# Performance work log

Hardware: AMD Instinct MI355X
Metric: run time of the kernel (lower is better)

Reference implementation:

```python
import jax, jax.numpy as jnp
import numpy as np

N, E, IN, H, NEX, NCAT = 100000, 1600000, 165, 128, 50, 3
EPS = 1e-5


def setup_inputs() -> dict:
    key = jax.random.key(0)
    ks = jax.random.split(key, 12)
    rn = lambda k, shp: (jax.random.normal(k, shp, jnp.float32) * 0.05)
    x = jax.random.normal(ks[0], (N, IN), jnp.float32)
    edge_index = jax.random.randint(ks[1], (2, E), 0, N, jnp.int32)
    inp = {
        'x': x, 'edge_index': edge_index,
        # GCN convs
        'W1': rn(ks[2], (IN, H)), 'b1': jnp.zeros((H,), jnp.float32),
        'W2': rn(ks[3], (H, H)), 'b2': jnp.zeros((H,), jnp.float32),
        # backbone BN (train-mode batch stats)
        'g1': jnp.ones((H,), jnp.float32), 'be1': jnp.zeros((H,), jnp.float32),
        'g2': jnp.ones((H,), jnp.float32), 'be2': jnp.zeros((H,), jnp.float32),
        # forward head
        'fW1': rn(ks[4], (H, H)), 'fb1': jnp.zeros((H,), jnp.float32),
        'fg1': jnp.ones((H,), jnp.float32), 'fbe1': jnp.zeros((H,), jnp.float32),
        'fW2': rn(ks[5], (H, H // 2)), 'fb2': jnp.zeros((H // 2,), jnp.float32),
        'fg2': jnp.ones((H // 2,), jnp.float32), 'fbe2': jnp.zeros((H // 2,), jnp.float32),
        'fW3': rn(ks[6], (H // 2, NEX)), 'fb3': jnp.zeros((NEX,), jnp.float32),
        # backward head
        'bW1': rn(ks[7], (H, H // 2)), 'bb1': jnp.zeros((H // 2,), jnp.float32),
        'bg1': jnp.ones((H // 2,), jnp.float32), 'bbe1': jnp.zeros((H // 2,), jnp.float32),
        'bW2': rn(ks[8], (H // 2, NCAT)), 'bb2': jnp.zeros((NCAT,), jnp.float32),
    }
    return inp


def _bn(h, g, b):
    # BatchNorm1d, training-mode stats (biased variance), dropout treated as identity
    m = h.mean(0)
    v = ((h - m) ** 2).mean(0)
    return (h - m) * jax.lax.rsqrt(v + EPS) * g + b


def _gcn(h, W, b, src, dst, dinv, n):
    h = h @ W                                   # [N, out]
    coef = (dinv[src] * dinv[dst])[:, None]     # sym-normalized edge weights
    msg = h[src] * coef                         # [E+N, out] gather
    out = jax.ops.segment_sum(msg, dst, num_segments=n)  # scatter-add
    return out + b


def reference(x, edge_index, W1, b1, W2, b2, g1, be1, g2, be2,
              fW1, fb1, fg1, fbe1, fW2, fb2, fg2, fbe2, fW3, fb3,
              bW1, bb1, bg1, bbe1, bW2, bb2):
    n = x.shape[0]
    loop = jnp.arange(n, dtype=edge_index.dtype)
    src = jnp.concatenate([edge_index[0], loop])  # add self-loops (PyG default)
    dst = jnp.concatenate([edge_index[1], loop])
    deg = jax.ops.segment_sum(jnp.ones(src.shape, x.dtype), dst, num_segments=n)
    dinv = jnp.where(deg > 0, jax.lax.rsqrt(jnp.maximum(deg, 1.0)), 0.0)

    h = jax.nn.relu(_bn(_gcn(x, W1, b1, src, dst, dinv, n), g1, be1))
    h = jax.nn.relu(_bn(_gcn(h, W2, b2, src, dst, dinv, n), g2, be2))
    emb = h

    f = jax.nn.relu(_bn(emb @ fW1 + fb1, fg1, fbe1))
    f = jax.nn.relu(_bn(f @ fW2 + fb2, fg2, fbe2))
    forward_logits = f @ fW3 + fb3

    bwd = jax.nn.relu(_bn(emb @ bW1 + bb1, bg1, bbe1))
    backward_logits = bwd @ bW2 + bb2

    return forward_logits, backward_logits, emb
```

## Files before the change

kernel.cpp:

```cpp
#include <hip/hip_runtime.h>
#include <stdint.h>

constexpr int NN = 100000;
constexpr int NE = 1600000;
constexpr int DIN = 165;
constexpr int PSZ = 12500;
constexpr int CAP = 48;

typedef __attribute__((ext_vector_type(8))) short bh8;
typedef __attribute__((ext_vector_type(4))) float f4;
typedef __attribute__((ext_vector_type(4))) float fx4;

__device__ inline unsigned short f2bf(float x) {
  union { float f; uint32_t u; } un; un.f = x;
  uint32_t u = un.u;
  return (unsigned short)((u + 0x7FFFu + ((u >> 16) & 1u)) >> 16);
}
__device__ inline float bf2f(unsigned short u) {
  union { uint32_t i; float f; } c; c.i = (uint32_t)u << 16; return c.f;
}
__device__ inline float bflo(uint32_t v) {
  union { uint32_t i; float f; } c; c.i = v << 16; return c.f;
}
__device__ inline float bfhi(uint32_t v) {
  union { uint32_t i; float f; } c; c.i = v & 0xffff0000u; return c.f;
}

__device__ inline f4 mfma16(bh8 a, bh8 b, f4 c) {
  return __builtin_amdgcn_mfma_f32_16x16x32_bf16(a, b, c, 0, 0, 0);
}

constexpr size_t OFF_DEG    = 0;
constexpr size_t OFF_STATS  = 400128;
constexpr size_t ZERO_BYTES = OFF_STATS + (size_t)5*64*256*4;
constexpr size_t OFF_DINV   = ZERO_BYTES;
constexpr size_t OFF_SS     = OFF_DINV + 400128;
constexpr size_t OFF_W1T    = OFF_SS + 5*256*4;
constexpr size_t OFF_W2T    = OFF_W1T + 128*192*2;
constexpr size_t OFF_FW1T   = OFF_W2T + 128*128*2;
constexpr size_t OFF_FW2T   = OFF_FW1T + 128*128*2;
constexpr size_t OFF_FW3T   = OFF_FW2T + 64*128*2;
constexpr size_t OFF_BW1T   = OFF_FW3T + 64*64*2;
constexpr size_t OFF_BW2T   = OFF_BW1T + 64*128*2;
constexpr size_t OFF_COL    = (OFF_BW2T + 16*64*2 + 255) & ~(size_t)255;
constexpr size_t OFF_BUF0   = (OFF_COL + (size_t)NN*CAP*4 + 255) & ~(size_t)255;
constexpr size_t OFF_BUF1   = OFF_BUF0 + (size_t)NN*128*2;
constexpr size_t OFF_BUF2   = OFF_BUF1 + (size_t)NN*128*2;

__global__ __launch_bounds__(256) void k_bfill(const int* __restrict__ srcv, const int* __restrict__ dstv,
                                               int* __restrict__ deg, int* __restrict__ colv) {
  int part = blockIdx.x & 7;
  int lo = part * PSZ, hi = lo + PSZ;
  const int4* s4 = (const int4*)srcv;
  const int4* d4 = (const int4*)dstv;
  constexpr int NQ = NE / 4;
  int stride = (gridDim.x >> 3) * 256;
#pragma unroll 2
  for (int q = (blockIdx.x >> 3) * 256 + threadIdx.x; q < NQ; q += stride) {
    int4 dd = d4[q];
    int4 ss = s4[q];
    if (dd.x >= lo && dd.x < hi) { int p = atomicAdd(&deg[dd.x], 1); if (p < CAP) colv[dd.x * CAP + p] = ss.x; }
    if (dd.y >= lo && dd.y < hi) { int p = atomicAdd(&deg[dd.y], 1); if (p < CAP) colv[dd.y * CAP + p] = ss.y; }
    if (dd.z >= lo && dd.z < hi) { int p = atomicAdd(&deg[dd.z], 1); if (p < CAP) colv[dd.z * CAP + p] = ss.z; }
    if (dd.w >= lo && dd.w < hi) { int p = atomicAdd(&deg[dd.w], 1); if (p < CAP) colv[dd.w * CAP + p] = ss.w; }
  }
}

__global__ __launch_bounds__(256) void k_prep(const float* __restrict__ W1, const float* __restrict__ W2,
                                              const float* __restrict__ fW1, const float* __restrict__ fW2,
                                              const float* __restrict__ fW3, const float* __restrict__ bW1,
                                              const float* __restrict__ bW2, char* __restrict__ wsb,
                                              const int* __restrict__ deg, float* __restrict__ dinv) {
  int b = blockIdx.x, t = threadIdx.x;
  if (b >= 308) {
    int i = (b - 308) * 256 + t;
    if (i < NN) dinv[i] = rsqrtf((float)(deg[i] + 1));
    return;
  }
  const float* src; unsigned short* dst; int K, C, Kpad, base;
  if (b < 96)       { src = W1;  dst = (unsigned short*)(wsb + OFF_W1T);  K = DIN; C = 128; Kpad = 192; base = b; }
  else if (b < 160) { src = W2;  dst = (unsigned short*)(wsb + OFF_W2T);  K = 128; C = 128; Kpad = 128; base = b - 96; }
  else if (b < 224) { src = fW1; dst = (unsigned short*)(wsb + OFF_FW1T); K = 128; C = 128; Kpad = 128; base = b - 160; }
  else if (b < 256) { src = fW2; dst = (unsigned short*)(wsb + OFF_FW2T); K = 128; C = 64;  Kpad = 128; base = b - 224; }
  else if (b < 272) { src = fW3; dst = (unsigned short*)(wsb + OFF_FW3T); K = 64;  C = 50;  Kpad = 64;  base = b - 256; }
  else if (b < 304) { src = bW1; dst = (unsigned short*)(wsb + OFF_BW1T); K = 128; C = 64;  Kpad = 128; base = b - 272; }
  else              { src = bW2; dst = (unsigned short*)(wsb + OFF_BW2T); K = 64;  C = 3;   Kpad = 64;  base = b - 304; }
  int idx = base * 256 + t;
  int c = idx / Kpad, k = idx - c * Kpad;
  float v = (c < C && k < K) ? src[k * C + c] : 0.f;
  dst[idx] = f2bf(v);
}

__global__ __launch_bounds__(256) void k_gx(const float* __restrict__ x,
                                            const unsigned short* __restrict__ W1T,
                                            unsigned short* __restrict__ out) {
  constexpr int KL = 200;
  __shared__ __attribute__((aligned(16))) unsigned short Alds[64 * KL];
  int tid = threadIdx.x;
  int lane = tid & 63, wave = tid >> 6;
  int lr = lane & 15, lk = (lane >> 4) * 8;
  int rowbase = blockIdx.x * 64;

  bh8 bw[2][6];
#pragma unroll
  for (int ct = 0; ct < 2; ++ct)
#pragma unroll
    for (int kt = 0; kt < 6; ++kt)
      bw[ct][kt] = *(const bh8*)&W1T[((wave * 2 + ct) * 16 + lr) * 192 + kt * 32 + lk];

  size_t slab = (size_t)rowbase * DIN;
  long rem = (long)NN * DIN - (long)slab;
  int lim4 = rem >= 10560 ? 2640 : (int)(rem >> 2);
  for (int z = tid; z < 64 * (192 - DIN); z += 256) {
    int r = z / (192 - DIN), k = DIN + (z - r * (192 - DIN));
    Alds[r * KL + k] = 0;
  }
  float4 regs[11];
#pragma unroll
  for (int i = 0; i < 11; ++i) {
    int idx4 = tid + i * 256;
    if (idx4 < lim4) regs[i] = *(const float4*)(x + slab + (size_t)idx4 * 4);
  }
#pragma unroll
  for (int i = 0; i < 11; ++i) {
    int idx4 = tid + i * 256;
    if (idx4 < lim4) {
      int e = idx4 * 4;
      int r = e / DIN, k = e - r * DIN;
      float vv[4] = {regs[i].x, regs[i].y, regs[i].z, regs[i].w};
#pragma unroll
      for (int j = 0; j < 4; ++j) {
        Alds[r * KL + k] = f2bf(vv[j]);
        if (++k == DIN) { k = 0; ++r; }
      }
    }
  }
  __syncthreads();

  f4 acc[4][2] = {};
  for (int kt = 0; kt < 6; ++kt) {
    bh8 a[4];
#pragma unroll
    for (int rt = 0; rt < 4; ++rt)
      a[rt] = *(const bh8*)&Alds[(rt * 16 + lr) * KL + kt * 32 + lk];
#pragma unroll
    for (int rt = 0; rt < 4; ++rt) {
      acc[rt][0] = mfma16(a[rt], bw[0][kt], acc[rt][0]);
      acc[rt][1] = mfma16(a[rt], bw[1][kt], acc[rt][1]);
    }
  }
#pragma unroll
  for (int ct = 0; ct < 2; ++ct) {
    int c = (wave * 2 + ct) * 16 + lr;
#pragma unroll
    for (int rt = 0; rt < 4; ++rt) {
      int gr0 = rowbase + rt * 16 + (lane >> 4) * 4;
#pragma unroll
      for (int rg = 0; rg < 4; ++rg) {
        int gr = gr0 + rg;
        if (gr < NN) out[(size_t)gr * 128 + c] = f2bf(acc[rt][ct][rg]);
      }
    }
  }
}

template <int KPAD, int CPAD, bool OUTBF>
__global__ __launch_bounds__(256) void k_gemm(const unsigned short* __restrict__ in, int K, int C,
                                              const float* __restrict__ ss,
                                              const unsigned short* __restrict__ WT,
                                              const float* __restrict__ bias,
                                              void* __restrict__ out_, float* __restrict__ stats) {
  constexpr int KL = KPAD + 8;
  constexpr int NKT = KPAD / 32;
  constexpr int NCTW = (CPAD >= 64) ? CPAD / 64 : 1;
  __shared__ __attribute__((aligned(16))) unsigned short Alds[64 * KL];
  __shared__ float s_sum[128], s_sq[128], sss[256];
  int tid = threadIdx.x;
  int lane = tid & 63, wave = tid >> 6;
  int lr = lane & 15, lk = (lane >> 4) * 8;
  int rowbase = blockIdx.x * 64;
  if (stats && tid < 128) { s_sum[tid] = 0.f; s_sq[tid] = 0.f; }

  bh8 bw[NCTW][NKT];
#pragma unroll
  for (int ct = 0; ct < NCTW; ++ct) {
    int cg = (CPAD >= 64) ? (wave * NCTW + ct) : 0;
#pragma unroll
    for (int kt = 0; kt < NKT; ++kt)
      bw[ct][kt] = *(const bh8*)&WT[(cg * 16 + lr) * KPAD + kt * 32 + lk];
  }

  if (ss && tid < 256) sss[tid] = ss[tid];

  {
    constexpr int NL = (64 * KPAD / 8) / 256;
    bh8 vv[NL];
#pragma unroll
    for (int i = 0; i < NL; ++i) {
      int idx8 = tid + i * 256;
      int r = idx8 / (KPAD / 8);
      int k = (idx8 - r * (KPAD / 8)) * 8;
      int gr = rowbase + r;
      vv[i] = (gr < NN) ? *(const bh8*)(in + (size_t)gr * KPAD + k) : bh8{};
    }
    if (ss) __syncthreads();
#pragma unroll
    for (int i = 0; i < NL; ++i) {
      int idx8 = tid + i * 256;
      int r = idx8 / (KPAD / 8);
      int k = (idx8 - r * (KPAD / 8)) * 8;
      bh8 v = vv[i];
      if (ss) {
#pragma unroll
        for (int j = 0; j < 8; ++j) {
          float f = bf2f((unsigned short)v[j]);
          f = fmaxf(fmaf(f, sss[k + j], sss[128 + k + j]), 0.f);
          v[j] = (short)f2bf(f);
        }
      }
      *(bh8*)&Alds[r * KL + k] = v;
    }
  }
  __syncthreads();

  if constexpr (CPAD >= 64) {
    f4 acc[4][NCTW] = {};
    for (int kt = 0; kt < NKT; ++kt) {
      bh8 a[4];
#pragma unroll
      for (int rt = 0; rt < 4; ++rt)
        a[rt] = *(const bh8*)&Alds[(rt * 16 + lr) * KL + kt * 32 + lk];
#pragma unroll
      for (int rt = 0; rt < 4; ++rt)
#pragma unroll
        for (int ct = 0; ct < NCTW; ++ct)
          acc[rt][ct] = mfma16(a[rt], bw[ct][kt], acc[rt][ct]);
    }
#pragma unroll
    for (int ct = 0; ct < NCTW; ++ct) {
      int c = (wave * NCTW + ct) * 16 + lr;
      float bv = (bias != nullptr && c < C) ? bias[c] : 0.f;
      float cs = 0.f, cq = 0.f;
#pragma unroll
      for (int rt = 0; rt < 4; ++rt) {
        int gr0 = rowbase + rt * 16 + (lane >> 4) * 4;
#pragma unroll
        for (int rg = 0; rg < 4; ++rg) {
          int gr = gr0 + rg;
          if (gr < NN && c < C) {
            float v = acc[rt][ct][rg] + bv;
            if (OUTBF) {
              unsigned short ub = f2bf(v);
              ((unsigned short*)out_)[(size_t)gr * C + c] = ub;
              v = bf2f(ub);
            } else {
              ((float*)out_)[(size_t)gr * C + c] = v;
            }
            cs += v; cq += v * v;
          }
        }
      }
      if (stats && c < C) { atomicAdd(&s_sum[c], cs); atomicAdd(&s_sq[c], cq); }
    }
  } else {
    f4 acc = {};
    for (int kt = 0; kt < NKT; ++kt) {
      bh8 a = *(const bh8*)&Alds[(wave * 16 + lr) * KL + kt * 32 + lk];
      acc = mfma16(a, bw[0][kt], acc);
    }
    int r0 = rowbase + wave * 16 + (lane >> 4) * 4;
    int c = lr;
#pragma unroll
    for (int rg = 0; rg < 4; ++rg) {
      int gr = r0 + rg;
      if (gr < NN && c < C) {
        float v = acc[rg] + ((bias != nullptr) ? bias[c] : 0.f);
        if (OUTBF) ((unsigned short*)out_)[(size_t)gr * C + c] = f2bf(v);
        else       ((float*)out_)[(size_t)gr * C + c] = v;
      }
    }
  }
  if (stats) {
    __syncthreads();
    int slot = blockIdx.x & 63;
    if (tid < 128) {
      atomicAdd(&stats[slot * 256 + tid], s_sum[tid]);
      atomicAdd(&stats[slot * 256 + 128 + tid], s_sq[tid]);
    }
  }
}

__global__ __launch_bounds__(256) void k_agg(const unsigned short* __restrict__ t, const int* __restrict__ colv,
                                             const int* __restrict__ deg,
                                             const float* __restrict__ dinv, unsigned short* __restrict__ out,
                                             float* __restrict__ stats) {
  __shared__ float rs[8][64], rq[8][64];
  int tid = threadIdx.x;
  int lane = tid & 63, wave = tid >> 6;
  int lg = lane >> 5;
  int l = lane & 31;
  int p = blockIdx.x & 7;
  int half = p >> 2;
  int sub = p & 3;
  int g = blockIdx.x >> 3;
  int node = g * 32 + sub * 8 + wave * 2 + lg;
  int cb = half * 64 + l * 2;
  float a0 = 0.f, a1 = 0.f;
  if (node < NN) {
    float di = dinv[node];
    uint32_t sv = *(const uint32_t*)(t + (size_t)node * 128 + cb);
    a0 = di * di * bflo(sv); a1 = di * di * bfhi(sv);
    int start = node * CAP;
    int len = min(deg[node], CAP);
    for (int j0 = 0; j0 < len; j0 += 32) {
      int cnt = min(len - j0, 32);
      int id = 0; float dv = 0.f;
      if (l < cnt) { id = colv[start + j0 + l]; dv = dinv[id]; }
      int j = 0;
      for (; j + 8 <= cnt; j += 8) {
        int s[8]; float c[8]; uint32_t v[8];
#pragma unroll
        for (int u = 0; u < 8; ++u) { s[u] = __shfl(id, j + u, 32); c[u] = __shfl(dv, j + u, 32) * di; }
#pragma unroll
        for (int u = 0; u < 8; ++u) v[u] = *(const uint32_t*)(t + (size_t)s[u] * 128 + cb);
#pragma unroll
        for (int u = 0; u < 8; ++u) { a0 = fmaf(c[u], bflo(v[u]), a0); a1 = fmaf(c[u], bfhi(v[u]), a1); }
      }
      for (; j < cnt; ++j) {
        int s = __shfl(id, j, 32);
        float c = __shfl(dv, j, 32) * di;
        uint32_t v = *(const uint32_t*)(t + (size_t)s * 128 + cb);
        a0 = fmaf(c, bflo(v), a0); a1 = fmaf(c, bfhi(v), a1);
      }
    }
    unsigned short u0 = f2bf(a0), u1 = f2bf(a1);
    uint32_t pack = (uint32_t)u0 | ((uint32_t)u1 << 16);
    __builtin_nontemporal_store(pack, (uint32_t*)(out + (size_t)node * 128 + cb));
    a0 = bf2f(u0); a1 = bf2f(u1);
  }
  int grp = wave * 2 + lg;
  rs[grp][l * 2] = a0; rs[grp][l * 2 + 1] = a1;
  rq[grp][l * 2] = a0 * a0; rq[grp][l * 2 + 1] = a1 * a1;
  __syncthreads();
  if (tid < 64) {
    float s = 0.f, q = 0.f;
#pragma unroll
    for (int k = 0; k < 8; ++k) { s += rs[k][tid]; q += rq[k][tid]; }
    int slot = blockIdx.x & 63;
    atomicAdd(&stats[slot * 256 + half * 64 + tid], s);
    atomicAdd(&stats[slot * 256 + 128 + half * 64 + tid], q);
  }
}

__global__ __launch_bounds__(128) void k_finalize(const float* __restrict__ stats, const float* __restrict__ g,
                                                  const float* __restrict__ be, float* __restrict__ ssout, int C) {
  int c = threadIdx.x;
  if (c < C) {
    float s = 0.f, q = 0.f;
    for (int k = 0; k < 64; ++k) { s += stats[k * 256 + c]; q += stats[k * 256 + 128 + c]; }
    const float invN = 1.f / (float)NN;
    float mean = s * invN;
    float var = fmaxf(q * invN - mean * mean, 0.f);
    float scale = g[c] * rsqrtf(var + 1e-5f);
    ssout[c] = scale;
    ssout[128 + c] = be[c] - mean * scale;
  }
}

__global__ __launch_bounds__(256) void k_head(const unsigned short* __restrict__ a2h,
                                              const float* __restrict__ ss2,
                                              const unsigned short* __restrict__ FW1T,
                                              const unsigned short* __restrict__ BW1T,
                                              float* __restrict__ emb,
                                              unsigned short* __restrict__ f1,
                                              unsigned short* __restrict__ b1,
                                              float* __restrict__ statsF, float* __restrict__ statsB) {
  constexpr int KL = 136;
  __shared__ __attribute__((aligned(16))) unsigned short Elds[64 * KL];
  __shared__ float sF_sum[128], sF_sq[128], sB_sum[64], sB_sq[64], sss[256];
  int tid = threadIdx.x;
  int lane = tid & 63, wave = tid >> 6;
  int lr = lane & 15, lk = (lane >> 4) * 8;
  int rowbase = blockIdx.x * 64;
  if (tid < 128) { sF_sum[tid] = 0.f; sF_sq[tid] = 0.f; }
  if (tid < 64)  { sB_sum[tid] = 0.f; sB_sq[tid] = 0.f; }

  bh8 bwF[2][4], bwB[4];
#pragma unroll
  for (int ct = 0; ct < 2; ++ct)
#pragma unroll
    for (int kt = 0; kt < 4; ++kt)
      bwF[ct][kt] = *(const bh8*)&FW1T[((wave * 2 + ct) * 16 + lr) * 128 + kt * 32 + lk];
#pragma unroll
  for (int kt = 0; kt < 4; ++kt)
    bwB[kt] = *(const bh8*)&BW1T[(wave * 16 + lr) * 128 + kt * 32 + lk];

  sss[tid] = ss2[tid & 255];

  bh8 vv[4];
#pragma unroll
  for (int i = 0; i < 4; ++i) {
    int idx8 = tid + i * 256;
    int r = idx8 >> 4, k = (idx8 & 15) * 8;
    int gr = rowbase + r;
    vv[i] = (gr < NN) ? *(const bh8*)(a2h + (size_t)gr * 128 + k) : bh8{};
  }
  __syncthreads();
#pragma unroll
  for (int i = 0; i < 4; ++i) {
    int idx8 = tid + i * 256;
    int r = idx8 >> 4, k = (idx8 & 15) * 8;
    int gr = rowbase + r;
    bh8 v = vv[i];
    float f[8];
#pragma unroll
    for (int j = 0; j < 8; ++j) {
      f[j] = fmaxf(fmaf(bf2f((unsigned short)v[j]), sss[k + j], sss[128 + k + j]), 0.f);
      v[j] = (short)f2bf(f[j]);
    }
    *(bh8*)&Elds[r * KL + k] = v;
    if (gr < NN) {
      fx4 o0 = {f[0], f[1], f[2], f[3]};
      fx4 o1 = {f[4], f[5], f[6], f[7]};
      __builtin_nontemporal_store(o0, (fx4*)(emb + (size_t)gr * 128 + k));
      __builtin_nontemporal_store(o1, (fx4*)(emb + (size_t)gr * 128 + k + 4));
    }
  }
  __syncthreads();

  f4 accF[4][2] = {};
  f4 accB[4] = {};
  for (int kt = 0; kt < 4; ++kt) {
    bh8 a[4];
#pragma unroll
    for (int rt = 0; rt < 4; ++rt)
      a[rt] = *(const bh8*)&Elds[(rt * 16 + lr) * KL + kt * 32 + lk];
#pragma unroll
    for (int rt = 0; rt < 4; ++rt) {
      accF[rt][0] = mfma16(a[rt], bwF[0][kt], accF[rt][0]);
      accF[rt][1] = mfma16(a[rt], bwF[1][kt], accF[rt][1]);
      accB[rt]    = mfma16(a[rt], bwB[kt],    accB[rt]);
    }
  }

#pragma unroll
  for (int ct = 0; ct < 2; ++ct) {
    int c = (wave * 2 + ct) * 16 + lr;
    float cs = 0.f, cq = 0.f;
#pragma unroll
    for (int rt = 0; rt < 4; ++rt) {
      int gr0 = rowbase + rt * 16 + (lane >> 4) * 4;
#pragma unroll
      for (int rg = 0; rg < 4; ++rg) {
        int gr = gr0 + rg;
        if (gr < NN) {
          unsigned short ub = f2bf(accF[rt][ct][rg]);
          f1[(size_t)gr * 128 + c] = ub;
          float v = bf2f(ub);
          cs += v; cq += v * v;
        }
      }
    }
    atomicAdd(&sF_sum[c], cs); atomicAdd(&sF_sq[c], cq);
  }
  {
    int c = wave * 16 + lr;
    float cs = 0.f, cq = 0.f;
#pragma unroll
    for (int rt = 0; rt < 4; ++rt) {
      int gr0 = rowbase + rt * 16 + (lane >> 4) * 4;
#pragma unroll
      for (int rg = 0; rg < 4; ++rg) {
        int gr = gr0 + rg;
        if (gr < NN) {
          unsigned short ub = f2bf(accB[rt][rg]);
          b1[(size_t)gr * 64 + c] = ub;
          float v = bf2f(ub);
          cs += v; cq += v * v;
        }
      }
    }
    atomicAdd(&sB_sum[c], cs); atomicAdd(&sB_sq[c], cq);
  }
  __syncthreads();
  int slot = blockIdx.x & 63;
  if (tid < 128) {
    atomicAdd(&statsF[slot * 256 + tid], sF_sum[tid]);
    atomicAdd(&statsF[slot * 256 + 128 + tid], sF_sq[tid]);
  } else if (tid < 192) {
    int c = tid - 128;
    atomicAdd(&statsB[slot * 256 + c], sB_sum[c]);
    atomicAdd(&statsB[slot * 256 + 128 + c], sB_sq[c]);
  }
}

extern "C" void kernel_launch(void* const* d_in, const int* in_sizes, int n_in,
                              void* d_out, int out_size, void* d_ws, size_t ws_size,
                              hipStream_t stream) {
  (void)in_sizes; (void)n_in; (void)out_size; (void)ws_size;
  const float* x   = (const float*)d_in[0];
  const int*   ei  = (const int*)d_in[1];
  const float* W1  = (const float*)d_in[2];
  const float* W2  = (const float*)d_in[4];
  const float* g1  = (const float*)d_in[6];
  const float* be1 = (const float*)d_in[7];
  const float* g2  = (const float*)d_in[8];
  const float* be2 = (const float*)d_in[9];
  const float* fW1 = (const float*)d_in[10];
  const float* fg1 = (const float*)d_in[12];
  const float* fbe1= (const float*)d_in[13];
  const float* fW2 = (const float*)d_in[14];
  const float* fg2 = (const float*)d_in[16];
  const float* fbe2= (const float*)d_in[17];
  const float* fW3 = (const float*)d_in[18];
  const float* fb3 = (const float*)d_in[19];
  const float* bW1 = (const float*)d_in[20];
  const float* bg1 = (const float*)d_in[22];
  const float* bbe1= (const float*)d_in[23];
  const float* bW2 = (const float*)d_in[24];
  const float* bb2 = (const float*)d_in[25];

  float* outp = (float*)d_out;
  float* fl  = outp;
  float* bl  = outp + (size_t)NN * 50;
  float* emb = outp + (size_t)NN * 53;

  char* wsb = (char*)d_ws;
  int*   deg    = (int*)(wsb + OFF_DEG);
  float* stats  = (float*)(wsb + OFF_STATS);
  float* dinv   = (float*)(wsb + OFF_DINV);
  float* ssb    = (float*)(wsb + OFF_SS);
  const unsigned short* W1T  = (const unsigned short*)(wsb + OFF_W1T);
  const unsigned short* W2T  = (const unsigned short*)(wsb + OFF_W2T);
  const unsigned short* FW1T = (const unsigned short*)(wsb + OFF_FW1T);
  const unsigned short* FW2T = (const unsigned short*)(wsb + OFF_FW2T);
  const unsigned short* FW3T = (const unsigned short*)(wsb + OFF_FW3T);
  const unsigned short* BW1T = (const unsigned short*)(wsb + OFF_BW1T);
  const unsigned short* BW2T = (const unsigned short*)(wsb + OFF_BW2T);
  int*            colv = (int*)(wsb + OFF_COL);
  unsigned short* buf0 = (unsigned short*)(wsb + OFF_BUF0);
  unsigned short* buf1 = (unsigned short*)(wsb + OFF_BUF1);
  unsigned short* buf2 = (unsigned short*)(wsb + OFF_BUF2);
  unsigned short* b1   = buf2 + (size_t)NN * 64;

  const int GG = (NN + 63) / 64;
  const int GA = 25000;
  const int GP = 2048;

  hipMemsetAsync(d_ws, 0, ZERO_BYTES, stream);

  k_bfill<<<GP, 256, 0, stream>>>(ei, ei + NE, deg, colv);
  k_prep <<<699, 256, 0, stream>>>(W1, W2, fW1, fW2, fW3, bW1, bW2, wsb, deg, dinv);

  k_gx<<<GG, 256, 0, stream>>>(x, W1T, buf0);
  k_agg<<<GA, 256, 0, stream>>>(buf0, colv, deg, dinv, buf1, stats + 0 * 16384);
  k_finalize<<<1, 128, 0, stream>>>(stats + 0 * 16384, g1, be1, ssb + 0 * 256, 128);

  k_gemm<128, 128, true><<<GG, 256, 0, stream>>>(buf1, 128, 128, ssb + 0 * 256, W2T, nullptr, buf0, nullptr);
  k_agg<<<GA, 256, 0, stream>>>(buf0, colv, deg, dinv, buf1, stats + 1 * 16384);
  k_finalize<<<1, 128, 0, stream>>>(stats + 1 * 16384, g2, be2, ssb + 1 * 256, 128);

  k_head<<<GG, 256, 0, stream>>>(buf1, ssb + 1 * 256, FW1T, BW1T, emb, buf0, b1,
                                 stats + 2 * 16384, stats + 3 * 16384);
  k_finalize<<<1, 128, 0, stream>>>(stats + 2 * 16384, fg1, fbe1, ssb + 2 * 256, 128);
  k_finalize<<<1, 128, 0, stream>>>(stats + 3 * 16384, bg1, bbe1, ssb + 3 * 256, 64);

  k_gemm<128, 64, true><<<GG, 256, 0, stream>>>(buf0, 128, 64, ssb + 2 * 256, FW2T, nullptr, buf2, stats + 4 * 16384);
  k_finalize<<<1, 128, 0, stream>>>(stats + 4 * 16384, fg2, fbe2, ssb + 4 * 256, 64);
  k_gemm<64, 64, false><<<GG, 256, 0, stream>>>(buf2, 64, 50, ssb + 4 * 256, FW3T, fb3, fl, nullptr);

  k_gemm<64, 16, false><<<GG, 256, 0, stream>>>(b1, 64, 3, ssb + 3 * 256, BW2T, bb2, bl, nullptr);
}
```

Measured before the change: 371.0 us.

## Widen GCN aggregation gathers to 16-byte loads with 8-lane node groups

The aggregation kernel is restructured so that each node is handled by 8 lanes, and each lane gathers 16 bytes (8 bf16 channels) per neighbor, replacing 32 lanes doing 4-byte loads. Each block now covers 128 nodes per half instead of 32, the grid shrinks to match, and BN statistics are reduced with shared-memory atomics. The edge-bucketing kernel also switches to nontemporal vector loads. Wider per-lane gathers should cut the number of memory instructions and shuffles, at the cost of more registers and shared-atomic contention during the stats reduction.

New measurement: 658.0 us. 77.3% more time.

```diff
diff --git a/kernel.cpp b/kernel.cpp
--- a/kernel.cpp
+++ b/kernel.cpp
@@ -10,6 +10,8 @@
 typedef __attribute__((ext_vector_type(8))) short bh8;
 typedef __attribute__((ext_vector_type(4))) float f4;
 typedef __attribute__((ext_vector_type(4))) float fx4;
+typedef __attribute__((ext_vector_type(4))) int ix4;
+typedef __attribute__((ext_vector_type(4))) unsigned int ux4;
 
 __device__ inline unsigned short f2bf(float x) {
   union { float f; uint32_t u; } un; un.f = x;
@@ -51,18 +53,22 @@
                                                int* __restrict__ deg, int* __restrict__ colv) {
   int part = blockIdx.x & 7;
   int lo = part * PSZ, hi = lo + PSZ;
-  const int4* s4 = (const int4*)srcv;
-  const int4* d4 = (const int4*)dstv;
+  const ix4* s4 = (const ix4*)srcv;
+  const ix4* d4 = (const ix4*)dstv;
   constexpr int NQ = NE / 4;
   int stride = (gridDim.x >> 3) * 256;
 #pragma unroll 2
   for (int q = (blockIdx.x >> 3) * 256 + threadIdx.x; q < NQ; q += stride) {
-    int4 dd = d4[q];
-    int4 ss = s4[q];
-    if (dd.x >= lo && dd.x < hi) { int p = atomicAdd(&deg[dd.x], 1); if (p < CAP) colv[dd.x * CAP + p] = ss.x; }
-    if (dd.y >= lo && dd.y < hi) { int p = atomicAdd(&deg[dd.y], 1); if (p < CAP) colv[dd.y * CAP + p] = ss.y; }
-    if (dd.z >= lo && dd.z < hi) { int p = atomicAdd(&deg[dd.z], 1); if (p < CAP) colv[dd.z * CAP + p] = ss.z; }
-    if (dd.w >= lo && dd.w < hi) { int p = atomicAdd(&deg[dd.w], 1); if (p < CAP) colv[dd.w * CAP + p] = ss.w; }
+    ix4 dd = __builtin_nontemporal_load(d4 + q);
+    ix4 ss = __builtin_nontemporal_load(s4 + q);
+#pragma unroll
+    for (int u = 0; u < 4; ++u) {
+      int d = dd[u];
+      if (d >= lo && d < hi) {
+        int p = atomicAdd(&deg[d], 1);
+        if (p < CAP) colv[d * CAP + p] = ss[u];
+      }
+    }
   }
 }
 
@@ -294,61 +300,82 @@
                                              const int* __restrict__ deg,
                                              const float* __restrict__ dinv, unsigned short* __restrict__ out,
                                              float* __restrict__ stats) {
-  __shared__ float rs[8][64], rq[8][64];
+  __shared__ float s_sum[64], s_sq[64];
   int tid = threadIdx.x;
-  int lane = tid & 63, wave = tid >> 6;
-  int lg = lane >> 5;
-  int l = lane & 31;
-  int p = blockIdx.x & 7;
-  int half = p >> 2;
-  int sub = p & 3;
-  int g = blockIdx.x >> 3;
-  int node = g * 32 + sub * 8 + wave * 2 + lg;
-  int cb = half * 64 + l * 2;
-  float a0 = 0.f, a1 = 0.f;
+  int gi = tid >> 3;
+  int l = tid & 7;
+  int half = (blockIdx.x & 7) >> 2;
+  int sub = blockIdx.x & 3;
+  int node = (blockIdx.x >> 3) * 128 + sub * 32 + gi;
+  int cb = half * 64 + l * 8;
+  if (tid < 64) { s_sum[tid] = 0.f; s_sq[tid] = 0.f; }
+  __syncthreads();
+
+  float a[8] = {};
   if (node < NN) {
     float di = dinv[node];
-    uint32_t sv = *(const uint32_t*)(t + (size_t)node * 128 + cb);
-    a0 = di * di * bflo(sv); a1 = di * di * bfhi(sv);
+    ux4 sv = *(const ux4*)(t + (size_t)node * 128 + cb);
+    float dd = di * di;
+    a[0] = dd * bflo(sv[0]); a[1] = dd * bfhi(sv[0]);
+    a[2] = dd * bflo(sv[1]); a[3] = dd * bfhi(sv[1]);
+    a[4] = dd * bflo(sv[2]); a[5] = dd * bfhi(sv[2]);
+    a[6] = dd * bflo(sv[3]); a[7] = dd * bfhi(sv[3]);
     int start = node * CAP;
     int len = min(deg[node], CAP);
-    for (int j0 = 0; j0 < len; j0 += 32) {
-      int cnt = min(len - j0, 32);
+    int j0 = 0;
+    for (; j0 + 8 <= len; j0 += 8) {
+      int id = colv[start + j0 + l];
+      float dv = dinv[id];
+      int s[8]; float c[8]; ux4 v[8];
+#pragma unroll
+      for (int u = 0; u < 8; ++u) { s[u] = __shfl(id, u, 8); c[u] = __shfl(dv, u, 8) * di; }
+#pragma unroll
+      for (int u = 0; u < 8; ++u) v[u] = *(const ux4*)(t + (size_t)s[u] * 128 + cb);
+#pragma unroll
+      for (int u = 0; u < 8; ++u) {
+        a[0] = fmaf(c[u], bflo(v[u][0]), a[0]); a[1] = fmaf(c[u], bfhi(v[u][0]), a[1]);
+        a[2] = fmaf(c[u], bflo(v[u][1]), a[2]); a[3] = fmaf(c[u], bfhi(v[u][1]), a[3]);
+        a[4] = fmaf(c[u], bflo(v[u][2]), a[4]); a[5] = fmaf(c[u], bfhi(v[u][2]), a[5]);
+        a[6] = fmaf(c[u], bflo(v[u][3]), a[6]); a[7] = fmaf(c[u], bfhi(v[u][3]), a[7]);
+      }
+    }
+    int rem = len - j0;
+    if (rem > 0) {
       int id = 0; float dv = 0.f;
-      if (l < cnt) { id = colv[start + j0 + l]; dv = dinv[id]; }
-      int j = 0;
-      for (; j + 8 <= cnt; j += 8) {
-        int s[8]; float c[8]; uint32_t v[8];
-#pragma unroll
-        for (int u = 0; u < 8; ++u) { s[u] = __shfl(id, j + u, 32); c[u] = __shfl(dv, j + u, 32) * di; }
-#pragma unroll
-        for (int u = 0; u < 8; ++u) v[u] = *(const uint32_t*)(t + (size_t)s[u] * 128 + cb);
-#pragma unroll
-        for (int u = 0; u < 8; ++u) { a0 = fmaf(c[u], bflo(v[u]), a0); a1 = fmaf(c[u], bfhi(v[u]), a1); }
-      }
-      for (; j < cnt; ++j) {
-        int s = __shfl(id, j, 32);
-        float c = __shfl(dv, j, 32) * di;
-        uint32_t v = *(const uint32_t*)(t + (size_t)s * 128 + cb);
-        a0 = fmaf(c, bflo(v), a0); a1 = fmaf(c, bfhi(v), a1);
-      }
-    }
-    unsigned short u0 = f2bf(a0), u1 = f2bf(a1);
-    uint32_t pack = (uint32_t)u0 | ((uint32_t)u1 << 16);
-    __builtin_nontemporal_store(pack, (uint32_t*)(out + (size_t)node * 128 + cb));
-    a0 = bf2f(u0); a1 = bf2f(u1);
-  }
-  int grp = wave * 2 + lg;
-  rs[grp][l * 2] = a0; rs[grp][l * 2 + 1] = a1;
-  rq[grp][l * 2] = a0 * a0; rq[grp][l * 2 + 1] = a1 * a1;
+      if (l < rem) { id = colv[start + j0 + l]; dv = dinv[id]; }
+      int s[8]; float c[8]; ux4 v[8];
+#pragma unroll
+      for (int u = 0; u < 8; ++u) { s[u] = __shfl(id, u, 8); c[u] = __shfl(dv, u, 8) * di; }
+#pragma unroll
+      for (int u = 0; u < 8; ++u) if (u < rem) v[u] = *(const ux4*)(t + (size_t)s[u] * 128 + cb);
+#pragma unroll
+      for (int u = 0; u < 8; ++u) if (u < rem) {
+        a[0] = fmaf(c[u], bflo(v[u][0]), a[0]); a[1] = fmaf(c[u], bfhi(v[u][0]), a[1]);
+        a[2] = fmaf(c[u], bflo(v[u][1]), a[2]); a[3] = fmaf(c[u], bfhi(v[u][1]), a[3]);
+        a[4] = fmaf(c[u], bflo(v[u][2]), a[4]); a[5] = fmaf(c[u], bfhi(v[u][2]), a[5]);
+        a[6] = fmaf(c[u], bflo(v[u][3]), a[6]); a[7] = fmaf(c[u], bfhi(v[u][3]), a[7]);
+      }
+    }
+    unsigned short ub[8];
+    ux4 o;
+#pragma unroll
+    for (int i = 0; i < 4; ++i) {
+      ub[2 * i] = f2bf(a[2 * i]); ub[2 * i + 1] = f2bf(a[2 * i + 1]);
+      o[i] = (uint32_t)ub[2 * i] | ((uint32_t)ub[2 * i + 1] << 16);
+      a[2 * i] = bf2f(ub[2 * i]); a[2 * i + 1] = bf2f(ub[2 * i + 1]);
+    }
+    __builtin_nontemporal_store(o, (ux4*)(out + (size_t)node * 128 + cb));
+  }
+#pragma unroll
+  for (int i = 0; i < 8; ++i) {
+    atomicAdd(&s_sum[l * 8 + i], a[i]);
+    atomicAdd(&s_sq[l * 8 + i], a[i] * a[i]);
+  }
   __syncthreads();
   if (tid < 64) {
-    float s = 0.f, q = 0.f;
-#pragma unroll
-    for (int k = 0; k < 8; ++k) { s += rs[k][tid]; q += rq[k][tid]; }
     int slot = blockIdx.x & 63;
-    atomicAdd(&stats[slot * 256 + half * 64 + tid], s);
-    atomicAdd(&stats[slot * 256 + 128 + half * 64 + tid], q);
+    atomicAdd(&stats[slot * 256 + half * 64 + tid], s_sum[tid]);
+    atomicAdd(&stats[slot * 256 + 128 + half * 64 + tid], s_sq[tid]);
   }
 }
 
@@ -544,7 +571,7 @@
   unsigned short* b1   = buf2 + (size_t)NN * 64;
 
   const int GG = (NN + 63) / 64;
-  const int GA = 25000;
+  const int GA = ((NN + 127) / 128) * 8;
   const int GP = 2048;
 
   hipMemsetAsync(d_ws, 0, ZERO_BYTES, stream);
```
